# Performance work log

Measured on AMD Instinct MI355X. Metric: run time of the kernel, lower is better.

## Reference

```python
import jax, jax.numpy as jnp
import numpy as np

LN_EPS = 1e-5  # torch LayerNorm default


def layer_norm(x, g, b):
    m = jnp.mean(x, axis=-1, keepdims=True)
    v = jnp.mean((x - m) ** 2, axis=-1, keepdims=True)
    return (x - m) / jnp.sqrt(v + LN_EPS) * g + b


def scatter_mean(src, idx, n):
    # src: [E, h], idx: [E] -> [n, h], mean with count clamped to >= 1
    s = jax.ops.segment_sum(src, idx, num_segments=n)
    cnt = jax.ops.segment_sum(jnp.ones((src.shape[0],), src.dtype), idx, num_segments=n)
    return s / jnp.clip(cnt, 1.0)[:, None]


def setup_inputs() -> dict:
    key = jax.random.key(0)
    ks = jax.random.split(key, 16)
    N, C, E, h = 200000, 50000, 600000, 128

    def w(k, shape, fan_in):
        return (jax.random.normal(k, shape, jnp.float32) / np.float32(np.sqrt(fan_in)))

    ci = jax.random.randint(ks[2], (E,), 0, C)
    vi = jax.random.randint(ks[3], (E,), 0, N)
    return {
        "vh": jax.random.normal(ks[0], (N, h), jnp.float32),
        "ch": jax.random.normal(ks[1], (C, h), jnp.float32),
        "edge_index": jnp.stack([ci, vi]).astype(jnp.int64),
        "ew": jax.random.normal(ks[4], (E,), jnp.float32),
        "v2c_lin_w": w(ks[5], (h, h), h), "v2c_lin_b": jnp.zeros((h,), jnp.float32),
        "v2c_gate_w": w(ks[6], (h, 1), 1), "v2c_gate_b": jnp.zeros((h,), jnp.float32),
        "v2c_upd_w": w(ks[7], (h, 2 * h), 2 * h), "v2c_upd_b": jnp.zeros((h,), jnp.float32),
        "v2c_ln_g": jnp.ones((h,), jnp.float32), "v2c_ln_b": jnp.zeros((h,), jnp.float32),
        "c2v_lin_w": w(ks[8], (h, h), h), "c2v_lin_b": jnp.zeros((h,), jnp.float32),
        "c2v_gate_w": w(ks[9], (h, 1), 1), "c2v_gate_b": jnp.zeros((h,), jnp.float32),
        "c2v_upd_w": w(ks[10], (h, 2 * h), 2 * h), "c2v_upd_b": jnp.zeros((h,), jnp.float32),
        "c2v_ln_g": jnp.ones((h,), jnp.float32), "c2v_ln_b": jnp.zeros((h,), jnp.float32),
    }


def reference(vh, ch, edge_index, ew,
              v2c_lin_w, v2c_lin_b, v2c_gate_w, v2c_gate_b,
              v2c_upd_w, v2c_upd_b, v2c_ln_g, v2c_ln_b,
              c2v_lin_w, c2v_lin_b, c2v_gate_w, c2v_gate_b,
              c2v_upd_w, c2v_upd_b, c2v_ln_g, c2v_ln_b):
    ci, vi = edge_index[0], edge_index[1]
    e = ew[:, None]  # [E, 1]

    # var -> con
    gate = jax.nn.sigmoid(e @ v2c_gate_w.T + v2c_gate_b)          # [E, h]
    msg = (vh @ v2c_lin_w.T + v2c_lin_b)[vi] * gate               # gather + gate
    agg = scatter_mean(msg, ci, ch.shape[0])                      # [C, h]
    ch_new = jax.nn.relu(layer_norm(
        jnp.concatenate([agg, ch], -1) @ v2c_upd_w.T + v2c_upd_b,
        v2c_ln_g, v2c_ln_b))

    # con -> var (uses updated ch)
    gate = jax.nn.sigmoid(e @ c2v_gate_w.T + c2v_gate_b)
    msg = (ch_new @ c2v_lin_w.T + c2v_lin_b)[ci] * gate
    agg = scatter_mean(msg, vi, vh.shape[0])                      # [N, h]
    vh_new = jax.nn.relu(layer_norm(
        jnp.concatenate([agg, vh], -1) @ c2v_upd_w.T + c2v_upd_b,
        c2v_ln_g, c2v_ln_b))

    return vh_new, ch_new
```

## Files before the change

kernel.cpp:

```cpp
#include <hip/hip_runtime.h>

#define LN_EPS 1e-5f

typedef float f32x4 __attribute__((ext_vector_type(4)));
typedef short bf16x8 __attribute__((ext_vector_type(8)));
typedef unsigned short u16x4 __attribute__((ext_vector_type(4)));

__device__ __forceinline__ unsigned short f2bf(float f) {
  unsigned int u = __float_as_uint(f);
  u = (u + 0x7fffu + ((u >> 16) & 1u)) >> 16;
  return (unsigned short)u;
}
__device__ __forceinline__ float bf2f(unsigned short h) {
  return __uint_as_float((unsigned int)h << 16);
}
__device__ __forceinline__ float sigm(float x) {
  return 1.f / (1.f + __expf(-x));
}

__global__ __launch_bounds__(256) void cvt4_bf16(const float* __restrict__ a,
                                                 const float* __restrict__ b,
                                                 const float* __restrict__ c,
                                                 const float* __restrict__ d,
                                                 unsigned short* __restrict__ oa,
                                                 unsigned short* __restrict__ ob,
                                                 unsigned short* __restrict__ oc,
                                                 unsigned short* __restrict__ od) {
  int i = blockIdx.x * 256 + threadIdx.x;
  if (i < 16384) oa[i] = f2bf(a[i]);
  else if (i < 49152) ob[i - 16384] = f2bf(b[i - 16384]);
  else if (i < 65536) oc[i - 49152] = f2bf(c[i - 49152]);
  else if (i < 98304) od[i - 65536] = f2bf(d[i - 65536]);
}

__global__ __launch_bounds__(256) void hist2_rank(const int* __restrict__ ci,
                                                  const int* __restrict__ vi,
                                                  int* __restrict__ cntC,
                                                  int* __restrict__ cntV,
                                                  int* __restrict__ rankC,
                                                  int* __restrict__ rankV, int E) {
  int tid = blockIdx.x * 256 + threadIdx.x;
  int T = gridDim.x * 256;
  int e[4], c[4], v[4];
  bool ok[4];
#pragma unroll
  for (int i = 0; i < 4; ++i) {
    e[i] = tid + i * T;
    ok[i] = e[i] < E;
  }
#pragma unroll
  for (int i = 0; i < 4; ++i) if (ok[i]) c[i] = ci[e[i]];
#pragma unroll
  for (int i = 0; i < 4; ++i) if (ok[i]) v[i] = vi[e[i]];
  int rc[4], rv[4];
#pragma unroll
  for (int i = 0; i < 4; ++i) if (ok[i]) rc[i] = atomicAdd(&cntC[c[i]], 1);
#pragma unroll
  for (int i = 0; i < 4; ++i) if (ok[i]) rv[i] = atomicAdd(&cntV[v[i]], 1);
#pragma unroll
  for (int i = 0; i < 4; ++i) if (ok[i]) rankC[e[i]] = rc[i];
#pragma unroll
  for (int i = 0; i < 4; ++i) if (ok[i]) rankV[e[i]] = rv[i];
}

__global__ __launch_bounds__(256) void scan1(const int* __restrict__ cnt,
                                             int* __restrict__ off,
                                             int* __restrict__ bsum, int M) {
  __shared__ int s[256];
  int base = blockIdx.x * 1024 + threadIdx.x * 4;
  int v[4];
  int tot = 0;
#pragma unroll
  for (int i = 0; i < 4; ++i) {
    int idx = base + i;
    v[i] = (idx < M) ? cnt[idx] : 0;
    tot += v[i];
  }
  s[threadIdx.x] = tot;
  __syncthreads();
  for (int d = 1; d < 256; d <<= 1) {
    int t = (threadIdx.x >= d) ? s[threadIdx.x - d] : 0;
    __syncthreads();
    s[threadIdx.x] += t;
    __syncthreads();
  }
  int excl = s[threadIdx.x] - tot;
#pragma unroll
  for (int i = 0; i < 4; ++i) {
    int idx = base + i;
    if (idx < M) off[idx] = excl;
    excl += v[i];
  }
  if (threadIdx.x == 255) bsum[blockIdx.x] = s[255];
}

__global__ __launch_bounds__(256) void scan2(int* __restrict__ bsum, int nb) {
  __shared__ int s[256];
  __shared__ int carry;
  if (threadIdx.x == 0) carry = 0;
  __syncthreads();
  for (int base = 0; base < nb; base += 256) {
    int idx = base + threadIdx.x;
    int v = (idx < nb) ? bsum[idx] : 0;
    s[threadIdx.x] = v;
    __syncthreads();
    for (int d = 1; d < 256; d <<= 1) {
      int t = (threadIdx.x >= d) ? s[threadIdx.x - d] : 0;
      __syncthreads();
      s[threadIdx.x] += t;
      __syncthreads();
    }
    if (idx < nb) bsum[idx] = s[threadIdx.x] - v + carry;
    __syncthreads();
    if (threadIdx.x == 0) carry += s[255];
    __syncthreads();
  }
}

__global__ __launch_bounds__(256) void scan3(int* __restrict__ off,
                                             const int* __restrict__ bsum, int M, int E) {
  int idx = blockIdx.x * 256 + threadIdx.x;
  if (idx < M) off[idx] += bsum[idx >> 10];
  if (idx == M) off[M] = E;
}

__global__ __launch_bounds__(256) void scatter2_kernel(const int* __restrict__ ci,
                                                       const int* __restrict__ vi,
                                                       const float* __restrict__ ew,
                                                       const int* __restrict__ offC,
                                                       const int* __restrict__ offV,
                                                       const int* __restrict__ rankC,
                                                       const int* __restrict__ rankV,
                                                       int2* __restrict__ edataC,
                                                       int2* __restrict__ edataV, int E) {
  int tid = blockIdx.x * 256 + threadIdx.x;
  int T = gridDim.x * 256;
  int e[4], c[4], v[4], wb[4], rc[4], rv[4];
  bool ok[4];
#pragma unroll
  for (int i = 0; i < 4; ++i) {
    e[i] = tid + i * T;
    ok[i] = e[i] < E;
  }
#pragma unroll
  for (int i = 0; i < 4; ++i) if (ok[i]) c[i] = ci[e[i]];
#pragma unroll
  for (int i = 0; i < 4; ++i) if (ok[i]) v[i] = vi[e[i]];
#pragma unroll
  for (int i = 0; i < 4; ++i) if (ok[i]) wb[i] = __float_as_int(ew[e[i]]);
#pragma unroll
  for (int i = 0; i < 4; ++i) if (ok[i]) rc[i] = rankC[e[i]];
#pragma unroll
  for (int i = 0; i < 4; ++i) if (ok[i]) rv[i] = rankV[e[i]];
  int pc[4], pv[4];
#pragma unroll
  for (int i = 0; i < 4; ++i) if (ok[i]) pc[i] = offC[c[i]] + rc[i];
#pragma unroll
  for (int i = 0; i < 4; ++i) if (ok[i]) pv[i] = offV[v[i]] + rv[i];
#pragma unroll
  for (int i = 0; i < 4; ++i) if (ok[i]) edataC[pc[i]] = make_int2(v[i], wb[i]);
#pragma unroll
  for (int i = 0; i < 4; ++i) if (ok[i]) edataV[pv[i]] = make_int2(c[i], wb[i]);
}

__global__ __launch_bounds__(256) void seg_reduce(const int* __restrict__ off,
                                                  const int2* __restrict__ edata,
                                                  const float* __restrict__ gw,
                                                  const float* __restrict__ gb,
                                                  const unsigned short* __restrict__ src,
                                                  int srcStride,
                                                  unsigned short* __restrict__ out,
                                                  int outStride, int M) {
  int seg = blockIdx.x * 4 + (threadIdx.x >> 6);
  if (seg >= M) return;
  int j = threadIdx.x & 63;
  int start = off[seg], end = off[seg + 1];
  float gwa = gw[2 * j], gwb = gw[2 * j + 1];
  float gba = gb[2 * j], gbb = gb[2 * j + 1];
  float a0 = 0.f, a1 = 0.f;
  int p = start;
  for (; p + 4 <= end; p += 4) {
    int2 e0 = edata[p], e1 = edata[p + 1], e2 = edata[p + 2], e3 = edata[p + 3];
    unsigned int v0 = *reinterpret_cast<const unsigned int*>(&src[(size_t)e0.x * srcStride + 2 * j]);
    unsigned int v1 = *reinterpret_cast<const unsigned int*>(&src[(size_t)e1.x * srcStride + 2 * j]);
    unsigned int v2 = *reinterpret_cast<const unsigned int*>(&src[(size_t)e2.x * srcStride + 2 * j]);
    unsigned int v3 = *reinterpret_cast<const unsigned int*>(&src[(size_t)e3.x * srcStride + 2 * j]);
    float w0 = __int_as_float(e0.y), w1 = __int_as_float(e1.y);
    float w2 = __int_as_float(e2.y), w3 = __int_as_float(e3.y);
    a0 += bf2f((unsigned short)(v0 & 0xffff)) * sigm(w0 * gwa + gba)
        + bf2f((unsigned short)(v1 & 0xffff)) * sigm(w1 * gwa + gba)
        + bf2f((unsigned short)(v2 & 0xffff)) * sigm(w2 * gwa + gba)
        + bf2f((unsigned short)(v3 & 0xffff)) * sigm(w3 * gwa + gba);
    a1 += bf2f((unsigned short)(v0 >> 16)) * sigm(w0 * gwb + gbb)
        + bf2f((unsigned short)(v1 >> 16)) * sigm(w1 * gwb + gbb)
        + bf2f((unsigned short)(v2 >> 16)) * sigm(w2 * gwb + gbb)
        + bf2f((unsigned short)(v3 >> 16)) * sigm(w3 * gwb + gbb);
  }
  if (p + 2 <= end) {
    int2 e0 = edata[p], e1 = edata[p + 1];
    unsigned int v0 = *reinterpret_cast<const unsigned int*>(&src[(size_t)e0.x * srcStride + 2 * j]);
    unsigned int v1 = *reinterpret_cast<const unsigned int*>(&src[(size_t)e1.x * srcStride + 2 * j]);
    float w0 = __int_as_float(e0.y), w1 = __int_as_float(e1.y);
    a0 += bf2f((unsigned short)(v0 & 0xffff)) * sigm(w0 * gwa + gba)
        + bf2f((unsigned short)(v1 & 0xffff)) * sigm(w1 * gwa + gba);
    a1 += bf2f((unsigned short)(v0 >> 16)) * sigm(w0 * gwb + gbb)
        + bf2f((unsigned short)(v1 >> 16)) * sigm(w1 * gwb + gbb);
    p += 2;
  }
  if (p < end) {
    int2 e0 = edata[p];
    unsigned int v0 = *reinterpret_cast<const unsigned int*>(&src[(size_t)e0.x * srcStride + 2 * j]);
    float w0 = __int_as_float(e0.y);
    a0 += bf2f((unsigned short)(v0 & 0xffff)) * sigm(w0 * gwa + gba);
    a1 += bf2f((unsigned short)(v0 >> 16)) * sigm(w0 * gwb + gbb);
  }
  int cnt = end - start;
  float inv = 1.f / (float)(cnt > 1 ? cnt : 1);
  unsigned int packed = (unsigned int)f2bf(a0 * inv) | ((unsigned int)f2bf(a1 * inv) << 16);
  *reinterpret_cast<unsigned int*>(&out[(size_t)seg * outStride + 2 * j]) = packed;
}

template <int OS, bool WBF>
__global__ __launch_bounds__(512) void gemm_lin_reg(const float* __restrict__ X,
                                                    const unsigned short* __restrict__ Wbf,
                                                    const float* __restrict__ bias,
                                                    unsigned short* __restrict__ out,
                                                    unsigned short* __restrict__ bfdst,
                                                    int M) {
  __shared__ unsigned short Bs[128][136];
  const int tid = threadIdx.x;
  const int lane = tid & 63, wv = tid >> 6;
  const int lr = lane & 15, lg = lane >> 4;
  const int row0 = blockIdx.x * 128 + wv * 16;

  const int arow = row0 + lr;
  const bool rowok = arow < M;
  const float* xrow = X + (size_t)arow * 128;

  float4 x0[4], x1[4];
#pragma unroll
  for (int ks = 0; ks < 4; ++ks) {
    int kb = ks * 32 + lg * 8;
    if (rowok) {
      x0[ks] = *reinterpret_cast<const float4*>(xrow + kb);
      x1[ks] = *reinterpret_cast<const float4*>(xrow + kb + 4);
    } else {
      x0[ks] = make_float4(0.f, 0.f, 0.f, 0.f);
      x1[ks] = x0[ks];
    }
  }

#pragma unroll
  for (int it = 0; it < 4; ++it) {
    int q = tid + it * 512;
    int n = q >> 4, kq = (q & 15) * 8;
    *reinterpret_cast<bf16x8*>(&Bs[n][kq]) =
        *reinterpret_cast<const bf16x8*>(&Wbf[(size_t)n * 128 + kq]);
  }

  bf16x8 a[4];
#pragma unroll
  for (int ks = 0; ks < 4; ++ks) {
    a[ks] = (bf16x8){(short)f2bf(x0[ks].x), (short)f2bf(x0[ks].y),
                     (short)f2bf(x0[ks].z), (short)f2bf(x0[ks].w),
                     (short)f2bf(x1[ks].x), (short)f2bf(x1[ks].y),
                     (short)f2bf(x1[ks].z), (short)f2bf(x1[ks].w)};
    if (WBF && rowok)
      *reinterpret_cast<bf16x8*>(&bfdst[(size_t)arow * 256 + 128 + ks * 32 + lg * 8]) = a[ks];
  }
  __syncthreads();

  f32x4 acc[8];
#pragma unroll
  for (int nf = 0; nf < 8; ++nf) acc[nf] = (f32x4)(0.f);
#pragma unroll
  for (int ks = 0; ks < 4; ++ks) {
#pragma unroll
    for (int nf = 0; nf < 8; ++nf) {
      bf16x8 b = *reinterpret_cast<const bf16x8*>(&Bs[nf * 16 + lr][ks * 32 + lg * 8]);
      acc[nf] = __builtin_amdgcn_mfma_f32_16x16x32_bf16(a[ks], b, acc[nf], 0, 0, 0);
    }
  }

#pragma unroll
  for (int nf = 0; nf < 8; ++nf) {
    int col = nf * 16 + lr;
    float bv = bias[col];
#pragma unroll
    for (int reg = 0; reg < 4; ++reg) {
      int grow = row0 + lg * 4 + reg;
      if (grow < M) out[(size_t)grow * OS + col] = f2bf(acc[nf][reg] + bv);
    }
  }
}

template <bool CAT>
__global__ __launch_bounds__(512) void gemm_upd_reg(const unsigned short* __restrict__ Xa,
                                                    const float* __restrict__ base,
                                                    const unsigned short* __restrict__ Wbf,
                                                    const float* __restrict__ bias,
                                                    const float* __restrict__ lng,
                                                    const float* __restrict__ lnb,
                                                    float* __restrict__ out, int M) {
  __shared__ unsigned short Bs[128][136];
  const int tid = threadIdx.x;
  const int lane = tid & 63, wv = tid >> 6;
  const int lr = lane & 15, lg = lane >> 4;
  const int row0 = blockIdx.x * 128 + wv * 16;
  const int arow = row0 + lr;
  const bool rowok = arow < M;

  bf16x8 a[8];
  if constexpr (CAT) {
    const unsigned short* xr = Xa + (size_t)arow * 256;
#pragma unroll
    for (int ks = 0; ks < 8; ++ks)
      a[ks] = rowok ? *reinterpret_cast<const bf16x8*>(xr + ks * 32 + lg * 8) : (bf16x8)(short)0;
  } else {
    const unsigned short* ar = Xa + (size_t)arow * 128;
#pragma unroll
    for (int ks = 0; ks < 4; ++ks)
      a[ks] = rowok ? *reinterpret_cast<const bf16x8*>(ar + ks * 32 + lg * 8) : (bf16x8)(short)0;
    const float* br = base + (size_t)arow * 128;
#pragma unroll
    for (int ks = 4; ks < 8; ++ks) {
      float4 f0 = make_float4(0.f, 0.f, 0.f, 0.f), f1 = f0;
      if (rowok) {
        int kb = (ks - 4) * 32 + lg * 8;
        f0 = *reinterpret_cast<const float4*>(br + kb);
        f1 = *reinterpret_cast<const float4*>(br + kb + 4);
      }
      a[ks] = (bf16x8){(short)f2bf(f0.x), (short)f2bf(f0.y), (short)f2bf(f0.z), (short)f2bf(f0.w),
                       (short)f2bf(f1.x), (short)f2bf(f1.y), (short)f2bf(f1.z), (short)f2bf(f1.w)};
    }
  }

  auto stageW = [&](int kh) {
#pragma unroll
    for (int it = 0; it < 4; ++it) {
      int q = tid + it * 512;
      int n = q >> 4, kq = (q & 15) * 8;
      *reinterpret_cast<bf16x8*>(&Bs[n][kq]) =
          *reinterpret_cast<const bf16x8*>(&Wbf[(size_t)n * 256 + kh * 128 + kq]);
    }
  };

  f32x4 acc[8];
#pragma unroll
  for (int nf = 0; nf < 8; ++nf) acc[nf] = (f32x4)(0.f);

  stageW(0);
  __syncthreads();
#pragma unroll
  for (int ks = 0; ks < 4; ++ks) {
#pragma unroll
    for (int nf = 0; nf < 8; ++nf) {
      bf16x8 b = *reinterpret_cast<const bf16x8*>(&Bs[nf * 16 + lr][ks * 32 + lg * 8]);
      acc[nf] = __builtin_amdgcn_mfma_f32_16x16x32_bf16(a[ks], b, acc[nf], 0, 0, 0);
    }
  }
  __syncthreads();
  stageW(1);
  __syncthreads();
#pragma unroll
  for (int ks = 4; ks < 8; ++ks) {
#pragma unroll
    for (int nf = 0; nf < 8; ++nf) {
      bf16x8 b = *reinterpret_cast<const bf16x8*>(&Bs[nf * 16 + lr][(ks - 4) * 32 + lg * 8]);
      acc[nf] = __builtin_amdgcn_mfma_f32_16x16x32_bf16(a[ks], b, acc[nf], 0, 0, 0);
    }
  }

  float bv[8], gv[8], lv[8];
#pragma unroll
  for (int nf = 0; nf < 8; ++nf) {
    int col = nf * 16 + lr;
    bv[nf] = bias[col];
    gv[nf] = lng[col];
    lv[nf] = lnb[col];
  }
#pragma unroll
  for (int reg = 0; reg < 4; ++reg) {
    float z[8];
    float s = 0.f, q = 0.f;
#pragma unroll
    for (int nf = 0; nf < 8; ++nf) {
      z[nf] = acc[nf][reg] + bv[nf];
      s += z[nf];
      q += z[nf] * z[nf];
    }
#pragma unroll
    for (int m = 1; m < 16; m <<= 1) {
      s += __shfl_xor(s, m);
      q += __shfl_xor(q, m);
    }
    float mean = s * (1.f / 128.f);
    float var = q * (1.f / 128.f) - mean * mean;
    float rstd = rsqrtf(var + LN_EPS);
    int grow = row0 + lg * 4 + reg;
    if (grow < M) {
#pragma unroll
      for (int nf = 0; nf < 8; ++nf) {
        float y = (z[nf] - mean) * rstd * gv[nf] + lv[nf];
        out[(size_t)grow * 128 + nf * 16 + lr] = fmaxf(y, 0.f);
      }
    }
  }
}

extern "C" void kernel_launch(void* const* d_in, const int* in_sizes, int n_in,
                              void* d_out, int out_size, void* d_ws, size_t ws_size,
                              hipStream_t stream) {
  const float* vh = (const float*)d_in[0];
  const float* ch = (const float*)d_in[1];
  const int* ei = (const int*)d_in[2];
  const float* ew = (const float*)d_in[3];
  const float* v2c_lin_w = (const float*)d_in[4];
  const float* v2c_lin_b = (const float*)d_in[5];
  const float* v2c_gate_w = (const float*)d_in[6];
  const float* v2c_gate_b = (const float*)d_in[7];
  const float* v2c_upd_w = (const float*)d_in[8];
  const float* v2c_upd_b = (const float*)d_in[9];
  const float* v2c_ln_g = (const float*)d_in[10];
  const float* v2c_ln_b = (const float*)d_in[11];
  const float* c2v_lin_w = (const float*)d_in[12];
  const float* c2v_lin_b = (const float*)d_in[13];
  const float* c2v_gate_w = (const float*)d_in[14];
  const float* c2v_gate_b = (const float*)d_in[15];
  const float* c2v_upd_w = (const float*)d_in[16];
  const float* c2v_upd_b = (const float*)d_in[17];
  const float* c2v_ln_g = (const float*)d_in[18];
  const float* c2v_ln_b = (const float*)d_in[19];

  const int N = in_sizes[0] / 128;
  const int C = in_sizes[1] / 128;
  const int E = in_sizes[3];
  const int* ci = ei;
  const int* vi = ei + E;

  unsigned short* Xcat = (unsigned short*)d_ws;
  unsigned short* aggC = Xcat + (size_t)N * 256;
  unsigned short* wbf = aggC + (size_t)C * 128;
  unsigned short* wbfLinV = wbf;
  unsigned short* wbfUpdV = wbf + 16384;
  unsigned short* wbfLinC = wbf + 49152;
  unsigned short* wbfUpdC = wbf + 65536;
  int* offC = (int*)(wbf + 98304);
  int* offV = offC + (C + 1);
  size_t ofs = (size_t)((offV + (N + 1)) - (int*)d_ws);
  ofs = (ofs + 1) & ~(size_t)1;
  int2* edataC = (int2*)((int*)d_ws + ofs);
  int2* edataV = edataC + E;
  int* cntC = (int*)aggC;
  int* cntV = cntC + C;
  int* bsumS = cntV + N;
  int* rankC = bsumS + 1024;
  int* rankV = rankC + E;

  float* vhNew = (float*)d_out;
  float* chNew = (float*)d_out + (size_t)N * 128;

  cvt4_bf16<<<(98304 + 255) / 256, 256, 0, stream>>>(v2c_lin_w, v2c_upd_w, c2v_lin_w,
                                                     c2v_upd_w, wbfLinV, wbfUpdV, wbfLinC,
                                                     wbfUpdC);

  const int egrid4 = (E + 4 * 256 - 1) / (4 * 256);

  hipMemsetAsync(cntC, 0, (size_t)(C + N) * sizeof(int), stream);
  hist2_rank<<<egrid4, 256, 0, stream>>>(ci, vi, cntC, cntV, rankC, rankV, E);
  {
    int nb = (C + 1023) / 1024;
    scan1<<<nb, 256, 0, stream>>>(cntC, offC, bsumS, C);
    scan2<<<1, 256, 0, stream>>>(bsumS, nb);
    scan3<<<(C + 1 + 255) / 256, 256, 0, stream>>>(offC, bsumS, C, E);
  }
  {
    int nb = (N + 1023) / 1024;
    scan1<<<nb, 256, 0, stream>>>(cntV, offV, bsumS, N);
    scan2<<<1, 256, 0, stream>>>(bsumS, nb);
    scan3<<<(N + 1 + 255) / 256, 256, 0, stream>>>(offV, bsumS, N, E);
  }
  scatter2_kernel<<<egrid4, 256, 0, stream>>>(ci, vi, ew, offC, offV, rankC, rankV,
                                              edataC, edataV, E);

  gemm_lin_reg<256, true><<<(N + 127) / 128, 512, 0, stream>>>(vh, wbfLinV, v2c_lin_b,
                                                               Xcat, Xcat, N);
  seg_reduce<<<(C + 3) / 4, 256, 0, stream>>>(offC, edataC, v2c_gate_w, v2c_gate_b,
                                              Xcat, 256, aggC, 128, C);
  gemm_upd_reg<false><<<(C + 127) / 128, 512, 0, stream>>>(aggC, ch, wbfUpdV, v2c_upd_b,
                                                           v2c_ln_g, v2c_ln_b, chNew, C);

  unsigned short* tmpC = aggC;
  gemm_lin_reg<128, false><<<(C + 127) / 128, 512, 0, stream>>>(chNew, wbfLinC, c2v_lin_b,
                                                                tmpC, nullptr, C);
  seg_reduce<<<(N + 3) / 4, 256, 0, stream>>>(offV, edataV, c2v_gate_w, c2v_gate_b,
                                              tmpC, 128, Xcat, 256, N);
  gemm_upd_reg<true><<<(N + 127) / 128, 512, 0, stream>>>(Xcat, nullptr, wbfUpdC,
                                                          c2v_upd_b, c2v_ln_g, c2v_ln_b,
                                                          vhNew, N);
}
```

Baseline: 330.7 us.

## Merge preprocessing launches: fuse cvt+hist, batch both scans, overlap scatter with lin GEMM

Combines the weight bf16 conversion with the edge histogram into one launch. The C-side and V-side prefix scans now run together in three launches instead of six. The edge scatter shares a launch with the first linear GEMM via block-index partitioning, so the independent work runs concurrently. This targets launch overhead and idle tails between small kernels, at the cost of heterogeneous blocks sharing LDS allocation and register limits in the fused kernel.

After: 315.6 us. 4.6% less time.

```diff
diff --git a/kernel.cpp b/kernel.cpp
--- a/kernel.cpp
+++ b/kernel.cpp
@@ -18,29 +18,31 @@
   return 1.f / (1.f + __expf(-x));
 }
 
-__global__ __launch_bounds__(256) void cvt4_bf16(const float* __restrict__ a,
-                                                 const float* __restrict__ b,
-                                                 const float* __restrict__ c,
-                                                 const float* __restrict__ d,
-                                                 unsigned short* __restrict__ oa,
-                                                 unsigned short* __restrict__ ob,
-                                                 unsigned short* __restrict__ oc,
-                                                 unsigned short* __restrict__ od) {
-  int i = blockIdx.x * 256 + threadIdx.x;
-  if (i < 16384) oa[i] = f2bf(a[i]);
-  else if (i < 49152) ob[i - 16384] = f2bf(b[i - 16384]);
-  else if (i < 65536) oc[i - 49152] = f2bf(c[i - 49152]);
-  else if (i < 98304) od[i - 65536] = f2bf(d[i - 65536]);
-}
-
-__global__ __launch_bounds__(256) void hist2_rank(const int* __restrict__ ci,
-                                                  const int* __restrict__ vi,
-                                                  int* __restrict__ cntC,
-                                                  int* __restrict__ cntV,
-                                                  int* __restrict__ rankC,
-                                                  int* __restrict__ rankV, int E) {
-  int tid = blockIdx.x * 256 + threadIdx.x;
-  int T = gridDim.x * 256;
+__global__ __launch_bounds__(256) void cvt_hist(const float* __restrict__ wa,
+                                                const float* __restrict__ wb,
+                                                const float* __restrict__ wc,
+                                                const float* __restrict__ wd,
+                                                unsigned short* __restrict__ oa,
+                                                unsigned short* __restrict__ ob,
+                                                unsigned short* __restrict__ oc,
+                                                unsigned short* __restrict__ od,
+                                                const int* __restrict__ ci,
+                                                const int* __restrict__ vi,
+                                                int* __restrict__ cntC,
+                                                int* __restrict__ cntV,
+                                                int* __restrict__ rankC,
+                                                int* __restrict__ rankV, int E, int hgrid) {
+  if ((int)blockIdx.x < 384) {
+    int i = blockIdx.x * 256 + threadIdx.x;
+    if (i < 16384) oa[i] = f2bf(wa[i]);
+    else if (i < 49152) ob[i - 16384] = f2bf(wb[i - 16384]);
+    else if (i < 65536) oc[i - 49152] = f2bf(wc[i - 49152]);
+    else if (i < 98304) od[i - 65536] = f2bf(wd[i - 65536]);
+    return;
+  }
+  int hb = blockIdx.x - 384;
+  int tid = hb * 256 + threadIdx.x;
+  int T = hgrid * 256;
   int e[4], c[4], v[4];
   bool ok[4];
 #pragma unroll
@@ -63,11 +65,11 @@
   for (int i = 0; i < 4; ++i) if (ok[i]) rankV[e[i]] = rv[i];
 }
 
-__global__ __launch_bounds__(256) void scan1(const int* __restrict__ cnt,
-                                             int* __restrict__ off,
-                                             int* __restrict__ bsum, int M) {
-  __shared__ int s[256];
-  int base = blockIdx.x * 1024 + threadIdx.x * 4;
+__device__ __forceinline__ void scan1_body(const int* __restrict__ cnt,
+                                           int* __restrict__ off,
+                                           int* __restrict__ bsum, int M, int bid,
+                                           int* s) {
+  int base = bid * 1024 + threadIdx.x * 4;
   int v[4];
   int tot = 0;
 #pragma unroll
@@ -91,12 +93,28 @@
     if (idx < M) off[idx] = excl;
     excl += v[i];
   }
-  if (threadIdx.x == 255) bsum[blockIdx.x] = s[255];
-}
-
-__global__ __launch_bounds__(256) void scan2(int* __restrict__ bsum, int nb) {
+  if (threadIdx.x == 255) bsum[bid] = s[255];
+}
+
+__global__ __launch_bounds__(256) void scanA(const int* __restrict__ cntC,
+                                             int* __restrict__ offC,
+                                             int* __restrict__ bsC, int Mc,
+                                             const int* __restrict__ cntV,
+                                             int* __restrict__ offV,
+                                             int* __restrict__ bsV, int Mv, int nbC) {
+  __shared__ int s[256];
+  if ((int)blockIdx.x < nbC)
+    scan1_body(cntC, offC, bsC, Mc, blockIdx.x, s);
+  else
+    scan1_body(cntV, offV, bsV, Mv, blockIdx.x - nbC, s);
+}
+
+__global__ __launch_bounds__(256) void scanB(int* __restrict__ bsC, int nbC,
+                                             int* __restrict__ bsV, int nbV) {
   __shared__ int s[256];
   __shared__ int carry;
+  int* bsum = (blockIdx.x == 0) ? bsC : bsV;
+  int nb = (blockIdx.x == 0) ? nbC : nbV;
   if (threadIdx.x == 0) carry = 0;
   __syncthreads();
   for (int base = 0; base < nb; base += 256) {
@@ -117,50 +135,124 @@
   }
 }
 
-__global__ __launch_bounds__(256) void scan3(int* __restrict__ off,
-                                             const int* __restrict__ bsum, int M, int E) {
-  int idx = blockIdx.x * 256 + threadIdx.x;
-  if (idx < M) off[idx] += bsum[idx >> 10];
-  if (idx == M) off[M] = E;
-}
-
-__global__ __launch_bounds__(256) void scatter2_kernel(const int* __restrict__ ci,
-                                                       const int* __restrict__ vi,
-                                                       const float* __restrict__ ew,
-                                                       const int* __restrict__ offC,
-                                                       const int* __restrict__ offV,
-                                                       const int* __restrict__ rankC,
-                                                       const int* __restrict__ rankV,
-                                                       int2* __restrict__ edataC,
-                                                       int2* __restrict__ edataV, int E) {
-  int tid = blockIdx.x * 256 + threadIdx.x;
-  int T = gridDim.x * 256;
-  int e[4], c[4], v[4], wb[4], rc[4], rv[4];
-  bool ok[4];
-#pragma unroll
-  for (int i = 0; i < 4; ++i) {
-    e[i] = tid + i * T;
-    ok[i] = e[i] < E;
-  }
-#pragma unroll
-  for (int i = 0; i < 4; ++i) if (ok[i]) c[i] = ci[e[i]];
-#pragma unroll
-  for (int i = 0; i < 4; ++i) if (ok[i]) v[i] = vi[e[i]];
-#pragma unroll
-  for (int i = 0; i < 4; ++i) if (ok[i]) wb[i] = __float_as_int(ew[e[i]]);
-#pragma unroll
-  for (int i = 0; i < 4; ++i) if (ok[i]) rc[i] = rankC[e[i]];
-#pragma unroll
-  for (int i = 0; i < 4; ++i) if (ok[i]) rv[i] = rankV[e[i]];
-  int pc[4], pv[4];
-#pragma unroll
-  for (int i = 0; i < 4; ++i) if (ok[i]) pc[i] = offC[c[i]] + rc[i];
-#pragma unroll
-  for (int i = 0; i < 4; ++i) if (ok[i]) pv[i] = offV[v[i]] + rv[i];
-#pragma unroll
-  for (int i = 0; i < 4; ++i) if (ok[i]) edataC[pc[i]] = make_int2(v[i], wb[i]);
-#pragma unroll
-  for (int i = 0; i < 4; ++i) if (ok[i]) edataV[pv[i]] = make_int2(c[i], wb[i]);
+__global__ __launch_bounds__(256) void scanC(int* __restrict__ offC,
+                                             const int* __restrict__ bsC, int Mc,
+                                             int* __restrict__ offV,
+                                             const int* __restrict__ bsV, int Mv,
+                                             int E, int gC) {
+  if ((int)blockIdx.x < gC) {
+    int idx = blockIdx.x * 256 + threadIdx.x;
+    if (idx < Mc) offC[idx] += bsC[idx >> 10];
+    if (idx == Mc) offC[Mc] = E;
+  } else {
+    int idx = (blockIdx.x - gC) * 256 + threadIdx.x;
+    if (idx < Mv) offV[idx] += bsV[idx >> 10];
+    if (idx == Mv) offV[Mv] = E;
+  }
+}
+
+__global__ __launch_bounds__(512) void lin_scatter(
+    const float* __restrict__ X, const unsigned short* __restrict__ Wbf,
+    const float* __restrict__ bias, unsigned short* __restrict__ out,
+    unsigned short* __restrict__ bfdst, int M,
+    const int* __restrict__ ci, const int* __restrict__ vi,
+    const float* __restrict__ ew, const int* __restrict__ offC,
+    const int* __restrict__ offV, const int* __restrict__ rankC,
+    const int* __restrict__ rankV, int2* __restrict__ edataC,
+    int2* __restrict__ edataV, int E, int sgrid) {
+  __shared__ unsigned short Bs[128][136];
+  const int tid = threadIdx.x;
+
+  if ((int)blockIdx.x < sgrid) {
+    int gtid = blockIdx.x * 512 + tid;
+    int T = sgrid * 512;
+    int e[2], c[2], v[2], wb[2], rc[2], rv[2];
+    bool ok[2];
+#pragma unroll
+    for (int i = 0; i < 2; ++i) {
+      e[i] = gtid + i * T;
+      ok[i] = e[i] < E;
+    }
+#pragma unroll
+    for (int i = 0; i < 2; ++i) if (ok[i]) c[i] = ci[e[i]];
+#pragma unroll
+    for (int i = 0; i < 2; ++i) if (ok[i]) v[i] = vi[e[i]];
+#pragma unroll
+    for (int i = 0; i < 2; ++i) if (ok[i]) wb[i] = __float_as_int(ew[e[i]]);
+#pragma unroll
+    for (int i = 0; i < 2; ++i) if (ok[i]) rc[i] = rankC[e[i]];
+#pragma unroll
+    for (int i = 0; i < 2; ++i) if (ok[i]) rv[i] = rankV[e[i]];
+#pragma unroll
+    for (int i = 0; i < 2; ++i) if (ok[i]) edataC[offC[c[i]] + rc[i]] = make_int2(v[i], wb[i]);
+#pragma unroll
+    for (int i = 0; i < 2; ++i) if (ok[i]) edataV[offV[v[i]] + rv[i]] = make_int2(c[i], wb[i]);
+    return;
+  }
+
+  const int bid = blockIdx.x - sgrid;
+  const int lane = tid & 63, wv = tid >> 6;
+  const int lr = lane & 15, lg = lane >> 4;
+  const int row0 = bid * 128 + wv * 16;
+  const int arow = row0 + lr;
+  const bool rowok = arow < M;
+  const float* xrow = X + (size_t)arow * 128;
+
+  float4 x0[4], x1[4];
+#pragma unroll
+  for (int ks = 0; ks < 4; ++ks) {
+    int kb = ks * 32 + lg * 8;
+    if (rowok) {
+      x0[ks] = *reinterpret_cast<const float4*>(xrow + kb);
+      x1[ks] = *reinterpret_cast<const float4*>(xrow + kb + 4);
+    } else {
+      x0[ks] = make_float4(0.f, 0.f, 0.f, 0.f);
+      x1[ks] = x0[ks];
+    }
+  }
+
+#pragma unroll
+  for (int it = 0; it < 4; ++it) {
+    int q = tid + it * 512;
+    int n = q >> 4, kq = (q & 15) * 8;
+    *reinterpret_cast<bf16x8*>(&Bs[n][kq]) =
+        *reinterpret_cast<const bf16x8*>(&Wbf[(size_t)n * 128 + kq]);
+  }
+
+  bf16x8 a[4];
+#pragma unroll
+  for (int ks = 0; ks < 4; ++ks) {
+    a[ks] = (bf16x8){(short)f2bf(x0[ks].x), (short)f2bf(x0[ks].y),
+                     (short)f2bf(x0[ks].z), (short)f2bf(x0[ks].w),
+                     (short)f2bf(x1[ks].x), (short)f2bf(x1[ks].y),
+                     (short)f2bf(x1[ks].z), (short)f2bf(x1[ks].w)};
+    if (rowok)
+      *reinterpret_cast<bf16x8*>(&bfdst[(size_t)arow * 256 + 128 + ks * 32 + lg * 8]) = a[ks];
+  }
+  __syncthreads();
+
+  f32x4 acc[8];
+#pragma unroll
+  for (int nf = 0; nf < 8; ++nf) acc[nf] = (f32x4)(0.f);
+#pragma unroll
+  for (int ks = 0; ks < 4; ++ks) {
+#pragma unroll
+    for (int nf = 0; nf < 8; ++nf) {
+      bf16x8 b = *reinterpret_cast<const bf16x8*>(&Bs[nf * 16 + lr][ks * 32 + lg * 8]);
+      acc[nf] = __builtin_amdgcn_mfma_f32_16x16x32_bf16(a[ks], b, acc[nf], 0, 0, 0);
+    }
+  }
+
+#pragma unroll
+  for (int nf = 0; nf < 8; ++nf) {
+    int col = nf * 16 + lr;
+    float bv = bias[col];
+#pragma unroll
+    for (int reg = 0; reg < 4; ++reg) {
+      int grow = row0 + lg * 4 + reg;
+      if (grow < M) out[(size_t)grow * 256 + col] = f2bf(acc[nf][reg] + bv);
+    }
+  }
 }
 
 __global__ __launch_bounds__(256) void seg_reduce(const int* __restrict__ off,
@@ -220,19 +312,16 @@
   *reinterpret_cast<unsigned int*>(&out[(size_t)seg * outStride + 2 * j]) = packed;
 }
 
-template <int OS, bool WBF>
 __global__ __launch_bounds__(512) void gemm_lin_reg(const float* __restrict__ X,
                                                     const unsigned short* __restrict__ Wbf,
                                                     const float* __restrict__ bias,
                                                     unsigned short* __restrict__ out,
-                                                    unsigned short* __restrict__ bfdst,
                                                     int M) {
   __shared__ unsigned short Bs[128][136];
   const int tid = threadIdx.x;
   const int lane = tid & 63, wv = tid >> 6;
   const int lr = lane & 15, lg = lane >> 4;
   const int row0 = blockIdx.x * 128 + wv * 16;
-
   const int arow = row0 + lr;
   const bool rowok = arow < M;
   const float* xrow = X + (size_t)arow * 128;
@@ -249,7 +338,6 @@
       x1[ks] = x0[ks];
     }
   }
-
 #pragma unroll
   for (int it = 0; it < 4; ++it) {
     int q = tid + it * 512;
@@ -257,17 +345,13 @@
     *reinterpret_cast<bf16x8*>(&Bs[n][kq]) =
         *reinterpret_cast<const bf16x8*>(&Wbf[(size_t)n * 128 + kq]);
   }
-
   bf16x8 a[4];
 #pragma unroll
-  for (int ks = 0; ks < 4; ++ks) {
+  for (int ks = 0; ks < 4; ++ks)
     a[ks] = (bf16x8){(short)f2bf(x0[ks].x), (short)f2bf(x0[ks].y),
                      (short)f2bf(x0[ks].z), (short)f2bf(x0[ks].w),
                      (short)f2bf(x1[ks].x), (short)f2bf(x1[ks].y),
                      (short)f2bf(x1[ks].z), (short)f2bf(x1[ks].w)};
-    if (WBF && rowok)
-      *reinterpret_cast<bf16x8*>(&bfdst[(size_t)arow * 256 + 128 + ks * 32 + lg * 8]) = a[ks];
-  }
   __syncthreads();
 
   f32x4 acc[8];
@@ -281,7 +365,6 @@
       acc[nf] = __builtin_amdgcn_mfma_f32_16x16x32_bf16(a[ks], b, acc[nf], 0, 0, 0);
     }
   }
-
 #pragma unroll
   for (int nf = 0; nf < 8; ++nf) {
     int col = nf * 16 + lr;
@@ -289,7 +372,7 @@
 #pragma unroll
     for (int reg = 0; reg < 4; ++reg) {
       int grow = row0 + lg * 4 + reg;
-      if (grow < M) out[(size_t)grow * OS + col] = f2bf(acc[nf][reg] + bv);
+      if (grow < M) out[(size_t)grow * 128 + col] = f2bf(acc[nf][reg] + bv);
     }
   }
 }
@@ -453,46 +536,41 @@
   int2* edataV = edataC + E;
   int* cntC = (int*)aggC;
   int* cntV = cntC + C;
-  int* bsumS = cntV + N;
-  int* rankC = bsumS + 1024;
+  int* bsumC = cntV + N;
+  int* bsumV = bsumC + 512;
+  int* rankC = bsumV + 512;
   int* rankV = rankC + E;
 
   float* vhNew = (float*)d_out;
   float* chNew = (float*)d_out + (size_t)N * 128;
 
-  cvt4_bf16<<<(98304 + 255) / 256, 256, 0, stream>>>(v2c_lin_w, v2c_upd_w, c2v_lin_w,
-                                                     c2v_upd_w, wbfLinV, wbfUpdV, wbfLinC,
-                                                     wbfUpdC);
-
-  const int egrid4 = (E + 4 * 256 - 1) / (4 * 256);
+  const int hgrid = (E + 4 * 256 - 1) / (4 * 256);
+  const int sgrid = (E + 2 * 512 - 1) / (2 * 512);
+  const int nbC = (C + 1023) / 1024;
+  const int nbN = (N + 1023) / 1024;
+  const int gC = (C + 1 + 255) / 256;
+  const int gN = (N + 1 + 255) / 256;
 
   hipMemsetAsync(cntC, 0, (size_t)(C + N) * sizeof(int), stream);
-  hist2_rank<<<egrid4, 256, 0, stream>>>(ci, vi, cntC, cntV, rankC, rankV, E);
-  {
-    int nb = (C + 1023) / 1024;
-    scan1<<<nb, 256, 0, stream>>>(cntC, offC, bsumS, C);
-    scan2<<<1, 256, 0, stream>>>(bsumS, nb);
-    scan3<<<(C + 1 + 255) / 256, 256, 0, stream>>>(offC, bsumS, C, E);
-  }
-  {
-    int nb = (N + 1023) / 1024;
-    scan1<<<nb, 256, 0, stream>>>(cntV, offV, bsumS, N);
-    scan2<<<1, 256, 0, stream>>>(bsumS, nb);
-    scan3<<<(N + 1 + 255) / 256, 256, 0, stream>>>(offV, bsumS, N, E);
-  }
-  scatter2_kernel<<<egrid4, 256, 0, stream>>>(ci, vi, ew, offC, offV, rankC, rankV,
-                                              edataC, edataV, E);
-
-  gemm_lin_reg<256, true><<<(N + 127) / 128, 512, 0, stream>>>(vh, wbfLinV, v2c_lin_b,
-                                                               Xcat, Xcat, N);
+  cvt_hist<<<384 + hgrid, 256, 0, stream>>>(v2c_lin_w, v2c_upd_w, c2v_lin_w, c2v_upd_w,
+                                            wbfLinV, wbfUpdV, wbfLinC, wbfUpdC,
+                                            ci, vi, cntC, cntV, rankC, rankV, E, hgrid);
+
+  scanA<<<nbC + nbN, 256, 0, stream>>>(cntC, offC, bsumC, C, cntV, offV, bsumV, N, nbC);
+  scanB<<<2, 256, 0, stream>>>(bsumC, nbC, bsumV, nbN);
+  scanC<<<gC + gN, 256, 0, stream>>>(offC, bsumC, C, offV, bsumV, N, E, gC);
+
+  lin_scatter<<<sgrid + (N + 127) / 128, 512, 0, stream>>>(
+      vh, wbfLinV, v2c_lin_b, Xcat, Xcat, N,
+      ci, vi, ew, offC, offV, rankC, rankV, edataC, edataV, E, sgrid);
+
   seg_reduce<<<(C + 3) / 4, 256, 0, stream>>>(offC, edataC, v2c_gate_w, v2c_gate_b,
                                               Xcat, 256, aggC, 128, C);
   gemm_upd_reg<false><<<(C + 127) / 128, 512, 0, stream>>>(aggC, ch, wbfUpdV, v2c_upd_b,
                                                            v2c_ln_g, v2c_ln_b, chNew, C);
 
   unsigned short* tmpC = aggC;
-  gemm_lin_reg<128, false><<<(C + 127) / 128, 512, 0, stream>>>(chNew, wbfLinC, c2v_lin_b,
-                                                                tmpC, nullptr, C);
+  gemm_lin_reg<<<(C + 127) / 128, 512, 0, stream>>>(chNew, wbfLinC, c2v_lin_b, tmpC, C);
   seg_reduce<<<(N + 3) / 4, 256, 0, stream>>>(offV, edataV, c2v_gate_w, c2v_gate_b,
                                               tmpC, 128, Xcat, 256, N);
   gemm_upd_reg<true><<<(N + 127) / 128, 512, 0, stream>>>(Xcat, nullptr, wbfUpdC,
```
